# Kernel tuning notes

Measured on AMD Instinct MI355X. Metric: run time of the kernel, lower is better.

The kernel has to match this reference:

```python
import jax, jax.numpy as jnp
import numpy as np

ALPHA = 0.01  # leaky relu negative slope


def _leaky(x):
    return jnp.where(x >= 0, x, ALPHA * x)


def setup_inputs() -> dict:
    key = jax.random.key(0)
    ks = jax.random.split(key, 8)
    B, N, Fin, Fout = 2, 1024, 64, 32
    inp = jax.random.normal(ks[0], (B, N, Fin), dtype=jnp.float32)
    k = jax.random.normal(ks[1], (B, N, Fin), dtype=jnp.float32)
    v = jax.random.normal(ks[2], (B, N, Fin), dtype=jnp.float32)
    adj = jax.random.uniform(ks[3], (N, N), dtype=jnp.float32)
    W = jax.random.normal(ks[4], (Fin, Fout), dtype=jnp.float32) * 0.1
    Wk = jax.random.normal(ks[5], (Fin, Fout), dtype=jnp.float32) * 0.1
    Wv = jax.random.normal(ks[6], (Fin, Fout), dtype=jnp.float32) * 0.1
    a = jax.random.normal(ks[7], (2 * Fout, 1), dtype=jnp.float32) * 0.1
    return {"inp": inp, "k": k, "v": v, "adj": adj, "W": W, "Wk": Wk, "Wv": Wv, "a": a}


def reference(inp, k, v, adj, W, Wk, Wv, a):
    # Projections
    h = jnp.matmul(inp, W)   # [B, N, F]
    kk = jnp.matmul(k, Wk)   # [B, N, F]
    vv = jnp.matmul(v, Wv)   # [B, N, F]
    B, N, F = h.shape
    # Faithful replication of the original (buggy) concat along dim=1 + view.
    th = jnp.tile(h, (1, 1, N)).reshape(B, N * N, F)   # row m=i*N+j -> h[:, i]
    tk = jnp.tile(kk, (1, N, 1))                       # row m -> k[:, m % N]
    cat = jnp.concatenate([th, tk], axis=1)            # [B, 2*N*N, F]
    cat = cat.reshape(B, N, N, 2 * F)                  # row-major reinterp (matches torch .view)
    scores = _leaky(jnp.einsum('bijc,co->bij', cat, a))  # [B, N, N]
    att = jax.nn.softmax(scores, axis=-1)
    # dropout is identity (eval mode, p=0.0)
    out = jnp.matmul((att + adj[None, :, :]) * 0.5, vv)  # [B, N, F]
    return _leaky(out)  # concat=True path
```

## Files before the change

kernel.cpp:

```cpp
#include <hip/hip_runtime.h>


#define ALPHA 0.01f

__device__ __forceinline__ float leaky(float x){ return x >= 0.f ? x : ALPHA*x; }

__global__ __launch_bounds__(256) void k_proj(
    const float* __restrict__ inp, const float* __restrict__ kin,
    const float* __restrict__ vin, const float* __restrict__ W,
    const float* __restrict__ Wk,  const float* __restrict__ Wv,
    const float* __restrict__ a,
    float* __restrict__ vv, float* __restrict__ p,
    float* __restrict__ q1, float* __restrict__ q2)
{
    int tid  = threadIdx.x;
    int lane = tid & 63;
    int f    = lane & 31;
    int h    = lane >> 5;
    int rl   = tid >> 6;
    int row  = blockIdx.x*4 + rl;
    const float* xr = inp + row*64 + h*32;
    const float* kr = kin + row*64 + h*32;
    const float* vr = vin + row*64 + h*32;
    const float* Wb  = W  + (h*32)*32 + f;
    const float* Wkb = Wk + (h*32)*32 + f;
    const float* Wvb = Wv + (h*32)*32 + f;
    float ha = 0.f, ka = 0.f, va = 0.f;
    #pragma unroll
    for (int c = 0; c < 32; c++){
        float x = xr[c], k = kr[c], v = vr[c];
        ha += x * Wb [c*32];
        ka += k * Wkb[c*32];
        va += v * Wvb[c*32];
    }
    ha += __shfl_xor(ha, 32);
    ka += __shfl_xor(ka, 32);
    va += __shfl_xor(va, 32);
    if (h == 0) vv[row*32 + f] = va;
    float a1 = a[f], a2 = a[32+f];
    float pv  = ha*(a1+a2);
    float q1v = ka*a1;
    float q2v = ka*a2;
    #pragma unroll
    for (int m = 16; m; m >>= 1){
        pv  += __shfl_xor(pv , m);
        q1v += __shfl_xor(q1v, m);
        q2v += __shfl_xor(q2v, m);
    }
    if (lane == 0){ p[row] = pv; q1[row] = q1v; q2[row] = q2v; }
}

__global__ __launch_bounds__(256) void k_fused(
    const float* __restrict__ adj, const float* __restrict__ vv,
    const float* __restrict__ p,   const float* __restrict__ q1,
    const float* __restrict__ q2,  float* __restrict__ out)
{
    __shared__ float e[1024];
    __shared__ float accred[4][4][32];
    __shared__ float xred[4][32];
    __shared__ float zred[4];

    int tid = threadIdx.x;
    int b   = blockIdx.x & 1;
    int it  = blockIdx.x >> 1;
    int o   = tid & 7;
    int rr  = (tid >> 3) & 3;
    int js  = tid >> 5;
    int w   = tid >> 6;
    int i   = it*4 + rr;
    bool hi = (it >= 128);

    const float4* ap = (const float4*)(adj + i*1024 + js*128);
    const float*  vb = vv + b*32768 + js*128*32 + o*4;
    float4 acc = make_float4(0.f,0.f,0.f,0.f);
    float4 aux = make_float4(0.f,0.f,0.f,0.f);

    if (hi){
        const float* q1b = q1 + b*1024;
        const float* q2b = q2 + b*1024;
        float zsum = 0.f;
        #pragma unroll
        for (int t = 0; t < 4; t++){
            int j  = tid*4 + t;
            float s = leaky(q1b[(2*j) & 1023] + q2b[(2*j+1) & 1023]);
            float ev = __expf(s);
            e[j] = ev;
            zsum += ev;
        }
        #pragma unroll
        for (int m = 32; m; m >>= 1) zsum += __shfl_xor(zsum, m);
        if ((tid & 63) == 0) zred[w] = zsum;
        __syncthreads();

        const float4* ep = (const float4*)(e + js*128);
        #pragma unroll 4
        for (int m = 0; m < 32; m++){
            float4 a4 = ap[m];
            float4 e4 = ep[m];
            const float* v0p = vb + m*128;
            float4 v0 = *(const float4*)(v0p);
            float4 v1 = *(const float4*)(v0p + 32);
            float4 v2 = *(const float4*)(v0p + 64);
            float4 v3 = *(const float4*)(v0p + 96);
            acc.x += a4.x*v0.x; acc.y += a4.x*v0.y; acc.z += a4.x*v0.z; acc.w += a4.x*v0.w;
            acc.x += a4.y*v1.x; acc.y += a4.y*v1.y; acc.z += a4.y*v1.z; acc.w += a4.y*v1.w;
            acc.x += a4.z*v2.x; acc.y += a4.z*v2.y; acc.z += a4.z*v2.z; acc.w += a4.z*v2.w;
            acc.x += a4.w*v3.x; acc.y += a4.w*v3.y; acc.z += a4.w*v3.z; acc.w += a4.w*v3.w;
            aux.x += e4.x*v0.x; aux.y += e4.x*v0.y; aux.z += e4.x*v0.z; aux.w += e4.x*v0.w;
            aux.x += e4.y*v1.x; aux.y += e4.y*v1.y; aux.z += e4.y*v1.z; aux.w += e4.y*v1.w;
            aux.x += e4.z*v2.x; aux.y += e4.z*v2.y; aux.z += e4.z*v2.z; aux.w += e4.z*v2.w;
            aux.x += e4.w*v3.x; aux.y += e4.w*v3.y; aux.z += e4.w*v3.z; aux.w += e4.w*v3.w;
        }
    } else {
        #pragma unroll 4
        for (int m = 0; m < 32; m++){
            float4 a4 = ap[m];
            const float* v0p = vb + m*128;
            float4 v0 = *(const float4*)(v0p);
            float4 v1 = *(const float4*)(v0p + 32);
            float4 v2 = *(const float4*)(v0p + 64);
            float4 v3 = *(const float4*)(v0p + 96);
            acc.x += a4.x*v0.x; acc.y += a4.x*v0.y; acc.z += a4.x*v0.z; acc.w += a4.x*v0.w;
            acc.x += a4.y*v1.x; acc.y += a4.y*v1.y; acc.z += a4.y*v1.z; acc.w += a4.y*v1.w;
            acc.x += a4.z*v2.x; acc.y += a4.z*v2.y; acc.z += a4.z*v2.z; acc.w += a4.z*v2.w;
            acc.x += a4.w*v3.x; acc.y += a4.w*v3.y; acc.z += a4.w*v3.z; acc.w += a4.w*v3.w;
            aux.x += v0.x + v1.x + v2.x + v3.x;
            aux.y += v0.y + v1.y + v2.y + v3.y;
            aux.z += v0.z + v1.z + v2.z + v3.z;
            aux.w += v0.w + v1.w + v2.w + v3.w;
        }
    }

    acc.x += __shfl_xor(acc.x, 32); acc.y += __shfl_xor(acc.y, 32);
    acc.z += __shfl_xor(acc.z, 32); acc.w += __shfl_xor(acc.w, 32);
    aux.x += __shfl_xor(aux.x, 32); aux.y += __shfl_xor(aux.y, 32);
    aux.z += __shfl_xor(aux.z, 32); aux.w += __shfl_xor(aux.w, 32);
    if ((tid & 32) == 0){
        accred[w][rr][o*4+0] = acc.x;
        accred[w][rr][o*4+1] = acc.y;
        accred[w][rr][o*4+2] = acc.z;
        accred[w][rr][o*4+3] = acc.w;
        if (rr == 0){
            xred[w][o*4+0] = aux.x; xred[w][o*4+1] = aux.y;
            xred[w][o*4+2] = aux.z; xred[w][o*4+3] = aux.w;
        }
    }
    __syncthreads();

    if (tid < 128){
        int rr2 = tid >> 5, f = tid & 31;
        float accsum = accred[0][rr2][f] + accred[1][rr2][f]
                     + accred[2][rr2][f] + accred[3][rr2][f];
        int i2 = it*4 + rr2;
        float att;
        if (!hi){
            float vlo = xred[0][f] + xred[1][f];
            float vhi = xred[2][f] + xred[3][f];
            float s0 = leaky(p[b*1024 + 2*i2]);
            float s1 = leaky(p[b*1024 + 2*i2 + 1]);
            float e0 = __expf(s0), e1 = __expf(s1);
            att = (e0*vlo + e1*vhi) / (512.f*(e0 + e1));
        } else {
            float rsum = xred[0][f] + xred[1][f] + xred[2][f] + xred[3][f];
            float Z = zred[0] + zred[1] + zred[2] + zred[3];
            att = rsum / Z;
        }
        out[(b*1024 + i2)*32 + f] = leaky(0.5f*(att + accsum));
    }
}

extern "C" void kernel_launch(void* const* d_in, const int* in_sizes, int n_in,
                              void* d_out, int out_size, void* d_ws, size_t ws_size,
                              hipStream_t stream)
{
    const float* inp = (const float*)d_in[0];
    const float* kin = (const float*)d_in[1];
    const float* vin = (const float*)d_in[2];
    const float* adj = (const float*)d_in[3];
    const float* W   = (const float*)d_in[4];
    const float* Wk  = (const float*)d_in[5];
    const float* Wv  = (const float*)d_in[6];
    const float* a   = (const float*)d_in[7];
    float* out = (float*)d_out;

    float* ws  = (float*)d_ws;
    float* vv  = ws;
    float* p   = ws + 65536;
    float* q1  = ws + 67584;
    float* q2  = ws + 69632;
    (void)in_sizes; (void)n_in; (void)out_size; (void)ws_size;

    hipLaunchKernelGGL(k_proj, dim3(512), dim3(256), 0, stream,
                       inp, kin, vin, W, Wk, Wv, a, vv, p, q1, q2);
    hipLaunchKernelGGL(k_fused, dim3(512), dim3(256), 0, stream,
                       adj, vv, p, q1, q2, out);
}
```

Baseline: 87.00 us.

## Fuse projection and attention kernels with per-batch flag barrier

Merges the projection kernel and the fused attention kernel into one launch. Each block publishes a release flag once its projection rows are written, then waits until all 256 blocks of its batch have published before starting the attention phase. This removes one kernel launch and the gap between the two kernels. The cost is spin-waiting, a dependence on all 512 blocks being co-resident, and a flag value derived from an uninitialised workspace word XORed with a constant. A stale flag that already matches this value could let a block start before the projections are done.

```diff
diff --git a/kernel.cpp b/kernel.cpp
--- a/kernel.cpp
+++ b/kernel.cpp
@@ -5,64 +5,80 @@
 
 __device__ __forceinline__ float leaky(float x){ return x >= 0.f ? x : ALPHA*x; }
 
-__global__ __launch_bounds__(256) void k_proj(
+__global__ __launch_bounds__(256) void k_gat(
     const float* __restrict__ inp, const float* __restrict__ kin,
     const float* __restrict__ vin, const float* __restrict__ W,
     const float* __restrict__ Wk,  const float* __restrict__ Wv,
-    const float* __restrict__ a,
+    const float* __restrict__ a,   const float* __restrict__ adj,
     float* __restrict__ vv, float* __restrict__ p,
-    float* __restrict__ q1, float* __restrict__ q2)
-{
-    int tid  = threadIdx.x;
-    int lane = tid & 63;
-    int f    = lane & 31;
-    int h    = lane >> 5;
-    int rl   = tid >> 6;
-    int row  = blockIdx.x*4 + rl;
-    const float* xr = inp + row*64 + h*32;
-    const float* kr = kin + row*64 + h*32;
-    const float* vr = vin + row*64 + h*32;
-    const float* Wb  = W  + (h*32)*32 + f;
-    const float* Wkb = Wk + (h*32)*32 + f;
-    const float* Wvb = Wv + (h*32)*32 + f;
-    float ha = 0.f, ka = 0.f, va = 0.f;
-    #pragma unroll
-    for (int c = 0; c < 32; c++){
-        float x = xr[c], k = kr[c], v = vr[c];
-        ha += x * Wb [c*32];
-        ka += k * Wkb[c*32];
-        va += v * Wvb[c*32];
-    }
-    ha += __shfl_xor(ha, 32);
-    ka += __shfl_xor(ka, 32);
-    va += __shfl_xor(va, 32);
-    if (h == 0) vv[row*32 + f] = va;
-    float a1 = a[f], a2 = a[32+f];
-    float pv  = ha*(a1+a2);
-    float q1v = ka*a1;
-    float q2v = ka*a2;
-    #pragma unroll
-    for (int m = 16; m; m >>= 1){
-        pv  += __shfl_xor(pv , m);
-        q1v += __shfl_xor(q1v, m);
-        q2v += __shfl_xor(q2v, m);
-    }
-    if (lane == 0){ p[row] = pv; q1[row] = q1v; q2[row] = q2v; }
-}
-
-__global__ __launch_bounds__(256) void k_fused(
-    const float* __restrict__ adj, const float* __restrict__ vv,
-    const float* __restrict__ p,   const float* __restrict__ q1,
-    const float* __restrict__ q2,  float* __restrict__ out)
+    float* __restrict__ q1, float* __restrict__ q2,
+    unsigned int* __restrict__ flags, const unsigned int* __restrict__ probe,
+    float* __restrict__ out)
 {
     __shared__ float e[1024];
     __shared__ float accred[4][4][32];
     __shared__ float xred[4][32];
     __shared__ float zred[4];
 
-    int tid = threadIdx.x;
-    int b   = blockIdx.x & 1;
-    int it  = blockIdx.x >> 1;
+    const int tid = threadIdx.x;
+    const int x   = blockIdx.x;
+
+    const unsigned int P     = probe[0];
+    const unsigned int magic = P ^ 0xA5A5A5A5u;
+
+    {
+        int lane = tid & 63;
+        int f    = lane & 31;
+        int h    = lane >> 5;
+        int rl   = tid >> 6;
+        int row  = x*4 + rl;
+        const float* xr = inp + row*64 + h*32;
+        const float* kr = kin + row*64 + h*32;
+        const float* vr = vin + row*64 + h*32;
+        const float* Wb  = W  + (h*32)*32 + f;
+        const float* Wkb = Wk + (h*32)*32 + f;
+        const float* Wvb = Wv + (h*32)*32 + f;
+        float ha = 0.f, ka = 0.f, va = 0.f;
+        #pragma unroll
+        for (int c = 0; c < 32; c++){
+            float xv = xr[c], kv = kr[c], vvl = vr[c];
+            ha += xv  * Wb [c*32];
+            ka += kv  * Wkb[c*32];
+            va += vvl * Wvb[c*32];
+        }
+        ha += __shfl_xor(ha, 32);
+        ka += __shfl_xor(ka, 32);
+        va += __shfl_xor(va, 32);
+        if (h == 0) vv[row*32 + f] = va;
+        float a1 = a[f], a2 = a[32+f];
+        float pv  = ha*(a1+a2);
+        float q1v = ka*a1;
+        float q2v = ka*a2;
+        #pragma unroll
+        for (int m = 16; m; m >>= 1){
+            pv  += __shfl_xor(pv , m);
+            q1v += __shfl_xor(q1v, m);
+            q2v += __shfl_xor(q2v, m);
+        }
+        if (lane == 0){ p[row] = pv; q1[row] = q1v; q2[row] = q2v; }
+    }
+
+    __syncthreads();
+    if (tid == 0){
+        __threadfence();
+        __hip_atomic_store(&flags[x], magic, __ATOMIC_RELEASE, __HIP_MEMORY_SCOPE_AGENT);
+    }
+
+    const int b  = x >> 8;
+    const int it = x & 255;
+
+    {
+        unsigned int* fb = flags + (b << 8);
+        while (__hip_atomic_load(&fb[tid], __ATOMIC_ACQUIRE, __HIP_MEMORY_SCOPE_AGENT) != magic)
+            __builtin_amdgcn_s_sleep(1);
+    }
+    __syncthreads();
+
     int o   = tid & 7;
     int rr  = (tid >> 3) & 3;
     int js  = tid >> 5;
@@ -188,10 +204,11 @@
     float* p   = ws + 65536;
     float* q1  = ws + 67584;
     float* q2  = ws + 69632;
+    unsigned int* flags = (unsigned int*)(ws + 73728);
+    const unsigned int* probe = (const unsigned int*)(ws + 81920);
     (void)in_sizes; (void)n_in; (void)out_size; (void)ws_size;
 
-    hipLaunchKernelGGL(k_proj, dim3(512), dim3(256), 0, stream,
-                       inp, kin, vin, W, Wk, Wv, a, vv, p, q1, q2);
-    hipLaunchKernelGGL(k_fused, dim3(512), dim3(256), 0, stream,
-                       adj, vv, p, q1, q2, out);
+    hipLaunchKernelGGL(k_gat, dim3(512), dim3(256), 0, stream,
+                       inp, kin, vin, W, Wk, Wv, a, adj,
+                       vv, p, q1, q2, flags, probe, out);
 }
```

Measured after the change: 137.4 us. +58.0%, slower.
